# Kernel optimization log

Measured on AMD Instinct MI355X. Metric: run time of the kernel, lower is better.

Reference implementation:

```python
import jax, jax.numpy as jnp
import numpy as np
import math

N = 50000          # n_nodes
E = 1600000        # n_edges (avg degree 32)
D = 256            # input_size
H = 8              # n_heads
HS = D // H        # head_size = 32


def setup_inputs() -> dict:
    key = jax.random.key(0)
    k1, k2, k3, k4, k5 = jax.random.split(key, 5)
    X = jax.random.normal(k1, (N, D), dtype=jnp.float32)
    # xavier_uniform for [D, HS] weight: bound = sqrt(6 / (fan_in + fan_out))
    bound = math.sqrt(6.0 / (D + HS))
    Wq = jax.random.uniform(k2, (D, HS), jnp.float32, -bound, bound)
    Wk = jax.random.uniform(k3, (D, HS), jnp.float32, -bound, bound)
    Wv = jax.random.uniform(k4, (D, HS), jnp.float32, -bound, bound)
    edge_index = jax.random.randint(k5, (2, E), 0, N, dtype=jnp.int32)
    return {"X": X, "Wq": Wq, "Wk": Wk, "Wv": Wv, "edge_index": edge_index}


def reference(X, Wq, Wk, Wv, edge_index):
    # Projections: [N, HS]
    Q = X @ Wq
    K = X @ Wk
    V = X @ Wv
    r = edge_index[0]  # row (query) node per edge
    c = edge_index[1]  # col (key/value) node per edge
    dk = jnp.asarray(math.sqrt(HS), dtype=X.dtype)
    # Edge-level attention logits: [E]
    scores = jnp.sum(Q[r] * K[c], axis=-1) / dk
    # Sparse row-wise (dim=1) softmax over existing edges only.
    row_max = jax.ops.segment_max(scores, r, num_segments=N)   # -inf for empty rows
    ex = jnp.exp(scores - row_max[r])                          # [E]
    denom = jax.ops.segment_sum(ex, r, num_segments=N)         # [N]
    # Weighted V aggregation: [N, HS]
    num = jax.ops.segment_sum(ex[:, None] * V[c], r, num_segments=N)
    # Rows with no incident edges produce zeros (matches sparse softmax + to_dense @ V).
    safe = jnp.maximum(denom, jnp.asarray(1e-30, X.dtype))[:, None]
    return jnp.where(denom[:, None] > 0, num / safe, jnp.zeros_like(num))
```

## Files before the change

### kernel.cpp

```cpp
#include <hip/hip_runtime.h>

#define N_NODES 50000
#define N_EDGES 1600000
#define D_IN    256
#define HS      32

#define NB      1250
#define ROWS_PB 40
#define CAP     1600
#define EPB     2048
#define BIN_B   ((N_EDGES + EPB - 1) / EPB)

#define MTILE   64
#define PROJ_B  ((N_NODES + MTILE - 1) / MTILE)
#define GRID_F  (PROJ_B + BIN_B)

typedef __bf16 bf16x8 __attribute__((ext_vector_type(8)));
typedef float  floatx4 __attribute__((ext_vector_type(4)));

static __device__ __forceinline__ unsigned short f2bf(float f) {
    unsigned u = __float_as_uint(f);
    return (unsigned short)((u + 0x7FFFu + ((u >> 16) & 1u)) >> 16);
}

__global__ __launch_bounds__(256) void wfrag_kernel(
    const float* __restrict__ Wq, const float* __restrict__ Wk,
    const float* __restrict__ Wv, unsigned short* __restrict__ wfrag)
{
    const int i = blockIdx.x * blockDim.x + threadIdx.x;
    if (i >= 8 * 6 * 64 * 8) return;
    const int j    = i & 7;
    const int lane = (i >> 3) & 63;
    const int st   = i >> 9;
    const int t    = st % 6;
    const int s    = st / 6;
    const int k    = s * 32 + (lane >> 4) * 8 + j;
    const int col  = t * 16 + (lane & 15);
    float v;
    if      (col < 32) v = Wq[k * HS + col];
    else if (col < 64) v = Wk[k * HS + (col - 32)];
    else               v = Wv[k * HS + (col - 64)];
    wfrag[i] = f2bf(v);
}

__global__ __launch_bounds__(256) void proj_bin_kernel(
    const float* __restrict__ X, const unsigned short* __restrict__ wfrag,
    float* __restrict__ Q, unsigned int* __restrict__ KVp,
    const int* __restrict__ er, const int* __restrict__ ec,
    int* __restrict__ fill, unsigned int* __restrict__ pairs)
{
    __shared__ int lcnt[NB];

    const int t = threadIdx.x;
    const int mod = blockIdx.x & 1;

    if (mod == 0) {
        const int pb = blockIdx.x >> 1;
        if (pb >= PROJ_B) return;
        const int lane = t & 63;
        const int w    = t >> 6;
        const int quad = lane >> 4;
        const int m16  = lane & 15;
        const int row0 = pb * MTILE;

        const int arow = w * 16 + m16;
        const int grc  = min(row0 + arow, N_NODES - 1);
        const float* xrow = X + (size_t)grc * D_IN;

        floatx4 acc[6];
#pragma unroll
        for (int nt = 0; nt < 6; nt++) acc[nt] = (floatx4)0.f;

#pragma unroll
        for (int s = 0; s < 8; s++) {
            const float4 a0 = *(const float4*)(xrow + s * 32 + quad * 8);
            const float4 a1 = *(const float4*)(xrow + s * 32 + quad * 8 + 4);
            union { bf16x8 v; unsigned short u[8]; } af;
            af.u[0] = f2bf(a0.x); af.u[1] = f2bf(a0.y);
            af.u[2] = f2bf(a0.z); af.u[3] = f2bf(a0.w);
            af.u[4] = f2bf(a1.x); af.u[5] = f2bf(a1.y);
            af.u[6] = f2bf(a1.z); af.u[7] = f2bf(a1.w);
            bf16x8 bfr[6];
#pragma unroll
            for (int nt = 0; nt < 6; nt++)
                bfr[nt] = *(const bf16x8*)(wfrag + (((s * 6 + nt) * 64 + lane) * 8));
#pragma unroll
            for (int nt = 0; nt < 6; nt++)
                acc[nt] = __builtin_amdgcn_mfma_f32_16x16x32_bf16(af.v, bfr[nt], acc[nt], 0, 0, 0);
        }

#pragma unroll
        for (int i = 0; i < 4; i++) {
            const int gr = row0 + w * 16 + quad * 4 + i;
            if (gr < N_NODES) {
#pragma unroll
                for (int nt = 0; nt < 2; nt++)
                    Q[gr * HS + nt * 16 + m16] = acc[nt][i];
#pragma unroll
                for (int p = 0; p < 2; p++) {
                    const int j = p * 16 + m16;
                    const unsigned kb = f2bf(acc[2 + p][i]);
                    const unsigned vb = f2bf(acc[4 + p][i]);
                    KVp[gr * HS + j] = (kb << 16) | vb;
                }
            }
        }
    } else {
        const int bb = blockIdx.x >> 1;
        const int e0 = bb * EPB;
        const int e1 = min(e0 + EPB, N_EDGES);

        for (int b = t; b < NB; b += 256) lcnt[b] = 0;
        __syncthreads();

        int rl[8], cl[8];
#pragma unroll
        for (int i = 0; i < 8; i++) {
            const int e = e0 + t + i * 256;
            if (e < e1) {
                rl[i] = er[e];
                cl[i] = ec[e];
                atomicAdd(&lcnt[rl[i] / ROWS_PB], 1);
            }
        }
        __syncthreads();

        for (int b = t; b < NB; b += 256) {
            const int c = lcnt[b];
            lcnt[b] = (c > 0) ? atomicAdd(&fill[b], c) : 0;
        }
        __syncthreads();

#pragma unroll
        for (int i = 0; i < 8; i++) {
            const int e = e0 + t + i * 256;
            if (e < e1) {
                const int r = rl[i];
                const int b = r / ROWS_PB;
                const int slot = atomicAdd(&lcnt[b], 1);
                pairs[(size_t)b * CAP + slot] =
                    ((unsigned)(r - b * ROWS_PB) << 16) | (unsigned)cl[i];
            }
        }
    }
}

__global__ __launch_bounds__(256) void bucket_agg_kernel(
    const unsigned int* __restrict__ pairs, const int* __restrict__ fill,
    const float* __restrict__ Q, const unsigned int* __restrict__ KVp,
    float* __restrict__ out)
{
    __shared__ unsigned srt[CAP];
    __shared__ int hist[4][ROWS_PB];
    __shared__ int sc[64];
    __shared__ int rowstart[ROWS_PB + 1];

    const int b = blockIdx.x;
    const int t = threadIdx.x;
    const int w = t >> 6;
    const int n = fill[b];
    const unsigned int* pbk = pairs + (size_t)b * CAP;

    for (int i = t; i < 4 * ROWS_PB; i += 256) ((int*)hist)[i] = 0;
    __syncthreads();

    unsigned pl[(CAP + 255) / 256];
#pragma unroll
    for (int k = 0; k < (CAP + 255) / 256; k++) {
        const int i = t + k * 256;
        if (i < n) {
            pl[k] = pbk[i];
            atomicAdd(&hist[w][pl[k] >> 16], 1);
        }
    }
    __syncthreads();

    if (t < 64)
        sc[t] = (t < ROWS_PB) ? (hist[0][t] + hist[1][t] + hist[2][t] + hist[3][t]) : 0;
    __syncthreads();
#pragma unroll
    for (int ofs = 1; ofs < 64; ofs <<= 1) {
        int u = 0;
        if (t < 64 && t >= ofs) u = sc[t - ofs];
        __syncthreads();
        if (t < 64) sc[t] += u;
        __syncthreads();
    }
    if (t < ROWS_PB) {
        const int h0 = hist[0][t], h1 = hist[1][t], h2 = hist[2][t], h3 = hist[3][t];
        const int excl = sc[t] - (h0 + h1 + h2 + h3);
        rowstart[t] = excl;
        int run = excl;
        hist[0][t] = run; run += h0;
        hist[1][t] = run; run += h1;
        hist[2][t] = run; run += h2;
        hist[3][t] = run;
    }
    if (t == 0) rowstart[ROWS_PB] = n;
    __syncthreads();

#pragma unroll
    for (int k = 0; k < (CAP + 255) / 256; k++) {
        const int i = t + k * 256;
        if (i < n) {
            const unsigned p = pl[k];
            const int pos = atomicAdd(&hist[w][p >> 16], 1);
            srt[pos] = p & 0xFFFFu;
        }
    }
    __syncthreads();

    const int lane = t & 63;
    const int comp = lane & 7;
    const int slot = lane >> 3;
    const float scale = 0.17677669529663687f;

#pragma unroll
    for (int rr = 0; rr < ROWS_PB / 4; rr++) {
        const int lr = w + rr * 4;
        const int gr = b * ROWS_PB + lr;
        const float4 q4 = *(const float4*)(Q + gr * HS + comp * 4);
        const int start = rowstart[lr];
        const int end   = rowstart[lr + 1];
        const int last  = end - 1;

        float accD = 0.f;
        float n0 = 0.f, n1 = 0.f, n2 = 0.f, n3 = 0.f;

        for (int e0 = start; e0 < end; e0 += 32) {
            int   cc[4];
            uint4 kv[4];
#pragma unroll
            for (int bb = 0; bb < 4; bb++)
                if (e0 + 8 * bb < end)
                    cc[bb] = (int)srt[min(e0 + 8 * bb + slot, last)];
#pragma unroll
            for (int bb = 0; bb < 4; bb++)
                if (e0 + 8 * bb < end)
                    kv[bb] = *(const uint4*)(KVp + (size_t)cc[bb] * HS + comp * 4);
#pragma unroll
            for (int bb = 0; bb < 4; bb++) {
                if (e0 + 8 * bb < end) {
                    float p = q4.x * __uint_as_float(kv[bb].x & 0xFFFF0000u)
                            + q4.y * __uint_as_float(kv[bb].y & 0xFFFF0000u)
                            + q4.z * __uint_as_float(kv[bb].z & 0xFFFF0000u)
                            + q4.w * __uint_as_float(kv[bb].w & 0xFFFF0000u);
#pragma unroll
                    for (int ofs = 1; ofs < 8; ofs <<= 1)
                        p += __shfl_xor(p, ofs, 64);
                    const float ex = (e0 + 8 * bb + slot < end) ? __expf(p * scale) : 0.f;
                    accD += ex;
                    n0 += ex * __uint_as_float(kv[bb].x << 16);
                    n1 += ex * __uint_as_float(kv[bb].y << 16);
                    n2 += ex * __uint_as_float(kv[bb].z << 16);
                    n3 += ex * __uint_as_float(kv[bb].w << 16);
                }
            }
        }

#pragma unroll
        for (int ofs = 8; ofs < 64; ofs <<= 1) {
            accD += __shfl_xor(accD, ofs, 64);
            n0 += __shfl_xor(n0, ofs, 64);
            n1 += __shfl_xor(n1, ofs, 64);
            n2 += __shfl_xor(n2, ofs, 64);
            n3 += __shfl_xor(n3, ofs, 64);
        }

        if (slot == 0) {
            const float inv = (accD > 0.f) ? 1.f / accD : 0.f;
            float4 o;
            o.x = n0 * inv; o.y = n1 * inv; o.z = n2 * inv; o.w = n3 * inv;
            *(float4*)(out + gr * HS + comp * 4) = o;
        }
    }
}

extern "C" void kernel_launch(void* const* d_in, const int* in_sizes, int n_in,
                              void* d_out, int out_size, void* d_ws, size_t ws_size,
                              hipStream_t stream)
{
    const float* X  = (const float*)d_in[0];
    const float* Wq = (const float*)d_in[1];
    const float* Wk = (const float*)d_in[2];
    const float* Wv = (const float*)d_in[3];
    const int*   ei = (const int*)d_in[4];
    const int* er = ei;
    const int* ec = ei + N_EDGES;

    float* out = (float*)d_out;

    float* Q          = (float*)d_ws;
    unsigned int* KVp = (unsigned int*)(Q + (size_t)N_NODES * HS);
    int* fill         = (int*)(KVp + (size_t)N_NODES * HS);
    unsigned short* wfrag = (unsigned short*)(fill + NB);
    unsigned int* pairs   = (unsigned int*)(wfrag + 8 * 6 * 64 * 8);

    hipMemsetAsync(fill, 0, NB * sizeof(int), stream);

    wfrag_kernel<<<(8 * 6 * 64 * 8 + 255) / 256, 256, 0, stream>>>(
        Wq, Wk, Wv, wfrag);

    proj_bin_kernel<<<GRID_F, 256, 0, stream>>>(
        X, wfrag, Q, KVp, er, ec, fill, pairs);

    bucket_agg_kernel<<<NB, 256, 0, stream>>>(pairs, fill, Q, KVp, out);
}
```

Before: 164.9 us.

## Merge projection and edge binning into each block, use direct global atomics

Each projection block now also bins a slice of about 2047 edges, so the separate binning blocks and their interleaved grid go away. The shared-memory two-phase local histogram with one global atomic per bucket is replaced by one global atomicAdd on the bucket fill counter per edge. This drops the LDS counters and block barriers, but sends 1.6M global atomics to only 1250 counters, which is likely to cause heavy contention. PROJ_B*2047 covers all edges, so correctness holds.

```diff
diff --git a/kernel.cpp b/kernel.cpp
--- a/kernel.cpp
+++ b/kernel.cpp
@@ -8,12 +8,10 @@
 #define NB      1250
 #define ROWS_PB 40
 #define CAP     1600
-#define EPB     2048
-#define BIN_B   ((N_EDGES + EPB - 1) / EPB)
 
 #define MTILE   64
 #define PROJ_B  ((N_NODES + MTILE - 1) / MTILE)
-#define GRID_F  (PROJ_B + BIN_B)
+#define EPPB    2047
 
 typedef __bf16 bf16x8 __attribute__((ext_vector_type(8)));
 typedef float  floatx4 __attribute__((ext_vector_type(4)));
@@ -49,14 +47,10 @@
     const int* __restrict__ er, const int* __restrict__ ec,
     int* __restrict__ fill, unsigned int* __restrict__ pairs)
 {
-    __shared__ int lcnt[NB];
-
-    const int t = threadIdx.x;
-    const int mod = blockIdx.x & 1;
-
-    if (mod == 0) {
-        const int pb = blockIdx.x >> 1;
-        if (pb >= PROJ_B) return;
+    const int t  = threadIdx.x;
+    const int pb = blockIdx.x;
+
+    {
         const int lane = t & 63;
         const int w    = t >> 6;
         const int quad = lane >> 4;
@@ -105,41 +99,21 @@
                 }
             }
         }
-    } else {
-        const int bb = blockIdx.x >> 1;
-        const int e0 = bb * EPB;
-        const int e1 = min(e0 + EPB, N_EDGES);
-
-        for (int b = t; b < NB; b += 256) lcnt[b] = 0;
-        __syncthreads();
-
-        int rl[8], cl[8];
-#pragma unroll
-        for (int i = 0; i < 8; i++) {
-            const int e = e0 + t + i * 256;
+    }
+
+    {
+        const int e0 = pb * EPPB;
+        const int e1 = min(e0 + EPPB, N_EDGES);
+#pragma unroll
+        for (int k = 0; k < 8; k++) {
+            const int e = e0 + t + k * 256;
             if (e < e1) {
-                rl[i] = er[e];
-                cl[i] = ec[e];
-                atomicAdd(&lcnt[rl[i] / ROWS_PB], 1);
-            }
-        }
-        __syncthreads();
-
-        for (int b = t; b < NB; b += 256) {
-            const int c = lcnt[b];
-            lcnt[b] = (c > 0) ? atomicAdd(&fill[b], c) : 0;
-        }
-        __syncthreads();
-
-#pragma unroll
-        for (int i = 0; i < 8; i++) {
-            const int e = e0 + t + i * 256;
-            if (e < e1) {
-                const int r = rl[i];
-                const int b = r / ROWS_PB;
-                const int slot = atomicAdd(&lcnt[b], 1);
-                pairs[(size_t)b * CAP + slot] =
-                    ((unsigned)(r - b * ROWS_PB) << 16) | (unsigned)cl[i];
+                const int r  = er[e];
+                const int c  = ec[e];
+                const int bk = r / ROWS_PB;
+                const int slot = atomicAdd(&fill[bk], 1);
+                pairs[(size_t)bk * CAP + slot] =
+                    ((unsigned)(r - bk * ROWS_PB) << 16) | (unsigned)c;
             }
         }
     }
@@ -301,7 +275,7 @@
     wfrag_kernel<<<(8 * 6 * 64 * 8 + 255) / 256, 256, 0, stream>>>(
         Wq, Wk, Wv, wfrag);
 
-    proj_bin_kernel<<<GRID_F, 256, 0, stream>>>(
+    proj_bin_kernel<<<PROJ_B, 256, 0, stream>>>(
         X, wfrag, Q, KVp, er, ec, fill, pairs);
 
     bucket_agg_kernel<<<NB, 256, 0, stream>>>(pairs, fill, Q, KVp, out);
```

Measured after the change: 417.4 us. 2.53x slower.
